# Optimization experiments

Hardware: AMD Instinct MI355X
Metric: run time of the kernel (lower is better)

The kernel has to match this reference:

```python
import jax, jax.numpy as jnp
import numpy as np
from jax import lax

T, I, H = 8192, 1024, 1024


def setup_inputs() -> dict:
    key = jax.random.key(0)
    ks = jax.random.split(key, 7)
    s = 1.0 / np.sqrt(H)
    x = jax.random.normal(ks[0], (T, I), dtype=jnp.float32)
    W_ih = jax.random.uniform(ks[1], (4 * H, I), minval=-s, maxval=s, dtype=jnp.float32)
    W_hh = jax.random.uniform(ks[2], (4 * H, H), minval=-s, maxval=s, dtype=jnp.float32)
    b_ih = jax.random.uniform(ks[3], (4 * H,), minval=-s, maxval=s, dtype=jnp.float32)
    b_hh = jax.random.uniform(ks[4], (4 * H,), minval=-s, maxval=s, dtype=jnp.float32)
    h0 = jax.random.normal(ks[5], (H,), dtype=jnp.float32)
    c0 = jax.random.uniform(ks[6], (H,), dtype=jnp.float32)
    return {"x": x, "W_ih": W_ih, "W_hh": W_hh, "b_ih": b_ih, "b_hh": b_hh, "h0": h0, "c0": c0}


def reference(x, W_ih, W_hh, b_ih, b_hh, h0, c0):
    # Precompute the input contribution to all gates in one big GEMM: [T, 4H]
    gates_x = x @ W_ih.T + (b_ih + b_hh)

    def step(carry, gx):
        h, c = carry
        g = gx + h @ W_hh.T  # [4H]
        i, f, gc, o = jnp.split(g, 4)  # PyTorch gate order: input, forget, cell, output
        i = jax.nn.sigmoid(i)
        f = jax.nn.sigmoid(f)
        gc = jnp.tanh(gc)
        o = jax.nn.sigmoid(o)
        c_new = f * c + i * gc
        h_new = o * jnp.tanh(c_new)
        return (h_new, c_new), h_new

    (_, _), hs = lax.scan(step, (h0, c0), gates_x)
    return hs  # [T, H] — the per-timestep outputs collected in fullDataOutput
```

## Files before the change

kernel.cpp:

```cpp
#include <hip/hip_runtime.h>
#include <cstdint>

#define T_STEPS 8192
#define HDIM    1024
#define NBLK    256
#define NTHR    256

typedef float        f32x4 __attribute__((ext_vector_type(4)));
typedef unsigned int u32x4 __attribute__((ext_vector_type(4)));

__device__ __forceinline__ float dot4(f32x4 a, f32x4 b) {
    return a[0] * b[0] + a[1] * b[1] + a[2] * b[2] + a[3] * b[3];
}
__device__ __forceinline__ float sigmoidf_(float v) { return 1.0f / (1.0f + __expf(-v)); }
__device__ __forceinline__ float tanhf_(float v)    { return 1.0f - 2.0f / (__expf(2.0f * v) + 1.0f); }
__device__ __forceinline__ unsigned bf16_rne(float f) {
    unsigned b = __float_as_uint(f);
    return (b + 0x7FFFu + ((b >> 16) & 1u)) >> 16;
}

__global__ __launch_bounds__(NTHR, 1)
void lstm_persistent(const float* __restrict__ x,
                     const float* __restrict__ W_ih,
                     const float* __restrict__ W_hh,
                     const float* __restrict__ b_ih,
                     const float* __restrict__ b_hh,
                     const float* __restrict__ h0,
                     const float* __restrict__ c0,
                     float* __restrict__ out,
                     unsigned int* __restrict__ ring)
{
    __shared__ float h_lds[2][HDIM];

    const int tid = threadIdx.x;
    const int w   = tid >> 6;
    const int l   = tid & 63;
    const int u   = (blockIdx.x << 2) + w;

    f32x4 whh[16], wih[16];
#pragma unroll
    for (int q = 0; q < 4; ++q) {
        const float* rh = W_hh + (size_t)(q * HDIM + u) * HDIM + 4 * l;
        const float* ri = W_ih + (size_t)(q * HDIM + u) * HDIM + 4 * l;
#pragma unroll
        for (int i = 0; i < 4; ++i) {
            whh[q * 4 + i] = *(const f32x4*)(rh + 256 * i);
            wih[q * 4 + i] = *(const f32x4*)(ri + 256 * i);
        }
    }
#pragma unroll
    for (int k = 0; k < 16; ++k) {
        asm volatile("" : "+v"(whh[k]));
        asm volatile("" : "+v"(wih[k]));
    }

    float bias[4];
#pragma unroll
    for (int q = 0; q < 4; ++q) bias[q] = b_ih[q * HDIM + u] + b_hh[q * HDIM + u];
    float c = c0[u];

    f32x4 hr[4];
#pragma unroll
    for (int i = 0; i < 4; ++i) hr[i] = *(const f32x4*)(h0 + 4 * l + 256 * i);

    float gxp[4];
    {
        f32x4 x0[4];
#pragma unroll
        for (int i = 0; i < 4; ++i) x0[i] = *(const f32x4*)(x + 4 * l + 256 * i);
#pragma unroll
        for (int q = 0; q < 4; ++q) {
            float a = 0.f;
#pragma unroll
            for (int i = 0; i < 4; ++i) a += dot4(wih[q * 4 + i], x0[i]);
            gxp[q] = a;
        }
    }
    f32x4 xr[4], xn[4];
#pragma unroll
    for (int i = 0; i < 4; ++i) xr[i] = *(const f32x4*)(x + HDIM + 4 * l + 256 * i);

    for (int t = 0; t < T_STEPS; ++t) {
        float acc[4];
#pragma unroll
        for (int q = 0; q < 4; ++q) {
            float a = gxp[q];
#pragma unroll
            for (int i = 0; i < 4; ++i) a += dot4(whh[q * 4 + i], hr[i]);
            acc[q] = a;
        }
#pragma unroll
        for (int m = 1; m < 64; m <<= 1) {
#pragma unroll
            for (int q = 0; q < 4; ++q) acc[q] += __shfl_xor(acc[q], m, 64);
        }
        const float gi = sigmoidf_(acc[0] + bias[0]);
        const float gf = sigmoidf_(acc[1] + bias[1]);
        const float gg = tanhf_   (acc[2] + bias[2]);
        const float go = sigmoidf_(acc[3] + bias[3]);
        c = gf * c + gi * gg;
        const float hval = go * tanhf_(c);

        if (l == 0) {
            const unsigned pk = ((unsigned)(t + 1) << 16) | bf16_rne(hval);
            unsigned int* slot =
                ring + (((t & 1) * NBLK + blockIdx.x) << 4) + w;
            asm volatile("global_store_dword %0, %1, off sc0 sc1"
                         :: "v"((unsigned long long)slot), "v"(pk) : "memory");
            out[(size_t)t * HDIM + u] = hval;
        }
        if (t == T_STEPS - 1) break;

        {
            const int tn = (t + 2 < T_STEPS) ? (t + 2) : (T_STEPS - 1);
            const float* xp = x + (size_t)tn * HDIM;
#pragma unroll
            for (int i = 0; i < 4; ++i) xn[i] = *(const f32x4*)(xp + 4 * l + 256 * i);
        }
#pragma unroll
        for (int q = 0; q < 4; ++q) {
            float a = 0.f;
#pragma unroll
            for (int i = 0; i < 4; ++i) a += dot4(wih[q * 4 + i], xr[i]);
            gxp[q] = a;
        }

        {
            const unsigned e = (unsigned)(t + 1);
            const unsigned long long base =
                (unsigned long long)(ring + (((t & 1) * NBLK + tid) << 4));
            u32x4 p;
            for (;;) {
                asm volatile(
                    "global_load_dwordx4 %0, %1, off sc0 sc1\n\t"
                    "s_waitcnt vmcnt(0)"
                    : "=&v"(p)
                    : "v"(base)
                    : "memory");
                if ((p[0] >> 16) == e && (p[1] >> 16) == e &&
                    (p[2] >> 16) == e && (p[3] >> 16) == e) break;
            }
            const int ns = (t + 1) & 1;
            f32x4 hv;
            hv[0] = __uint_as_float(p[0] << 16);
            hv[1] = __uint_as_float(p[1] << 16);
            hv[2] = __uint_as_float(p[2] << 16);
            hv[3] = __uint_as_float(p[3] << 16);
            *(f32x4*)&h_lds[ns][4 * tid] = hv;
        }
        __syncthreads();
        {
            const int ns = (t + 1) & 1;
#pragma unroll
            for (int i = 0; i < 4; ++i)
                hr[i] = *(const f32x4*)&h_lds[ns][4 * l + 256 * i];
        }
#pragma unroll
        for (int i = 0; i < 4; ++i) xr[i] = xn[i];
    }
}

extern "C" void kernel_launch(void* const* d_in, const int* in_sizes, int n_in,
                              void* d_out, int out_size, void* d_ws, size_t ws_size,
                              hipStream_t stream)
{
    const float* x    = (const float*)d_in[0];
    const float* W_ih = (const float*)d_in[1];
    const float* W_hh = (const float*)d_in[2];
    const float* b_ih = (const float*)d_in[3];
    const float* b_hh = (const float*)d_in[4];
    const float* h0   = (const float*)d_in[5];
    const float* c0   = (const float*)d_in[6];

    unsigned int* ring = (unsigned int*)d_ws;
    hipMemsetAsync(d_ws, 0, 2 * NBLK * 16 * sizeof(unsigned int), stream);
    lstm_persistent<<<NBLK, NTHR, 0, stream>>>(x, W_ih, W_hh, b_ih, b_hh, h0, c0,
                                               (float*)d_out, ring);
}
```

Measured before the change: 22.27 ms.

## Add dedicated polling wave per block to gather hidden state, overlapping compute waves

Adds a fifth wavefront to each block that alone polls the global ring buffer for the other blocks' hidden values, issuing four dwordx4 loads per lane and sleeping briefly between polls. The four compute waves no longer poll and only compute the input projection for the next step before the barrier. This separates synchronization latency from compute and aims to cut polling traffic from 256 threads to 64 per block. The output store moves to lane 1 so it does not share a lane with the ring store. The cost is an extra wave and a serial dependency on one polling wave, whose s_sleep may add latency on the critical path.

```diff
diff --git a/kernel.cpp b/kernel.cpp
--- a/kernel.cpp
+++ b/kernel.cpp
@@ -4,7 +4,7 @@
 #define T_STEPS 8192
 #define HDIM    1024
 #define NBLK    256
-#define NTHR    256
+#define NTHR    320
 
 typedef float        f32x4 __attribute__((ext_vector_type(4)));
 typedef unsigned int u32x4 __attribute__((ext_vector_type(4)));
@@ -38,125 +38,151 @@
     const int u   = (blockIdx.x << 2) + w;
 
     f32x4 whh[16], wih[16];
-#pragma unroll
-    for (int q = 0; q < 4; ++q) {
-        const float* rh = W_hh + (size_t)(q * HDIM + u) * HDIM + 4 * l;
-        const float* ri = W_ih + (size_t)(q * HDIM + u) * HDIM + 4 * l;
-#pragma unroll
-        for (int i = 0; i < 4; ++i) {
-            whh[q * 4 + i] = *(const f32x4*)(rh + 256 * i);
-            wih[q * 4 + i] = *(const f32x4*)(ri + 256 * i);
-        }
+    float bias[4] = {};
+    float c = 0.f;
+    f32x4 hr[4] = {};
+    float gxp[4] = {};
+    f32x4 xr[4] = {}, xn[4] = {};
+
+    if (w < 4) {
+#pragma unroll
+        for (int q = 0; q < 4; ++q) {
+            const float* rh = W_hh + (size_t)(q * HDIM + u) * HDIM + 4 * l;
+            const float* ri = W_ih + (size_t)(q * HDIM + u) * HDIM + 4 * l;
+#pragma unroll
+            for (int i = 0; i < 4; ++i) {
+                whh[q * 4 + i] = *(const f32x4*)(rh + 256 * i);
+                wih[q * 4 + i] = *(const f32x4*)(ri + 256 * i);
+            }
+        }
+#pragma unroll
+        for (int k = 0; k < 16; ++k) {
+            asm volatile("" : "+v"(whh[k]));
+            asm volatile("" : "+v"(wih[k]));
+        }
+#pragma unroll
+        for (int q = 0; q < 4; ++q) bias[q] = b_ih[q * HDIM + u] + b_hh[q * HDIM + u];
+        c = c0[u];
+#pragma unroll
+        for (int i = 0; i < 4; ++i) hr[i] = *(const f32x4*)(h0 + 4 * l + 256 * i);
+        {
+            f32x4 x0[4];
+#pragma unroll
+            for (int i = 0; i < 4; ++i) x0[i] = *(const f32x4*)(x + 4 * l + 256 * i);
+#pragma unroll
+            for (int q = 0; q < 4; ++q) {
+                float a = 0.f;
+#pragma unroll
+                for (int i = 0; i < 4; ++i) a += dot4(wih[q * 4 + i], x0[i]);
+                gxp[q] = a;
+            }
+        }
+#pragma unroll
+        for (int i = 0; i < 4; ++i) xr[i] = *(const f32x4*)(x + HDIM + 4 * l + 256 * i);
     }
-#pragma unroll
-    for (int k = 0; k < 16; ++k) {
-        asm volatile("" : "+v"(whh[k]));
-        asm volatile("" : "+v"(wih[k]));
-    }
-
-    float bias[4];
-#pragma unroll
-    for (int q = 0; q < 4; ++q) bias[q] = b_ih[q * HDIM + u] + b_hh[q * HDIM + u];
-    float c = c0[u];
-
-    f32x4 hr[4];
-#pragma unroll
-    for (int i = 0; i < 4; ++i) hr[i] = *(const f32x4*)(h0 + 4 * l + 256 * i);
-
-    float gxp[4];
-    {
-        f32x4 x0[4];
-#pragma unroll
-        for (int i = 0; i < 4; ++i) x0[i] = *(const f32x4*)(x + 4 * l + 256 * i);
-#pragma unroll
-        for (int q = 0; q < 4; ++q) {
-            float a = 0.f;
-#pragma unroll
-            for (int i = 0; i < 4; ++i) a += dot4(wih[q * 4 + i], x0[i]);
-            gxp[q] = a;
-        }
-    }
-    f32x4 xr[4], xn[4];
-#pragma unroll
-    for (int i = 0; i < 4; ++i) xr[i] = *(const f32x4*)(x + HDIM + 4 * l + 256 * i);
+
+    const unsigned long long ringb = (unsigned long long)ring;
 
     for (int t = 0; t < T_STEPS; ++t) {
-        float acc[4];
-#pragma unroll
-        for (int q = 0; q < 4; ++q) {
-            float a = gxp[q];
-#pragma unroll
-            for (int i = 0; i < 4; ++i) a += dot4(whh[q * 4 + i], hr[i]);
-            acc[q] = a;
-        }
-#pragma unroll
-        for (int m = 1; m < 64; m <<= 1) {
-#pragma unroll
-            for (int q = 0; q < 4; ++q) acc[q] += __shfl_xor(acc[q], m, 64);
-        }
-        const float gi = sigmoidf_(acc[0] + bias[0]);
-        const float gf = sigmoidf_(acc[1] + bias[1]);
-        const float gg = tanhf_   (acc[2] + bias[2]);
-        const float go = sigmoidf_(acc[3] + bias[3]);
-        c = gf * c + gi * gg;
-        const float hval = go * tanhf_(c);
-
-        if (l == 0) {
-            const unsigned pk = ((unsigned)(t + 1) << 16) | bf16_rne(hval);
-            unsigned int* slot =
-                ring + (((t & 1) * NBLK + blockIdx.x) << 4) + w;
-            asm volatile("global_store_dword %0, %1, off sc0 sc1"
-                         :: "v"((unsigned long long)slot), "v"(pk) : "memory");
-            out[(size_t)t * HDIM + u] = hval;
+        if (w < 4) {
+            float acc[4];
+#pragma unroll
+            for (int q = 0; q < 4; ++q) {
+                float a = gxp[q];
+#pragma unroll
+                for (int i = 0; i < 4; ++i) a += dot4(whh[q * 4 + i], hr[i]);
+                acc[q] = a;
+            }
+#pragma unroll
+            for (int m = 1; m < 64; m <<= 1) {
+#pragma unroll
+                for (int q = 0; q < 4; ++q) acc[q] += __shfl_xor(acc[q], m, 64);
+            }
+            const float gi = sigmoidf_(acc[0] + bias[0]);
+            const float gf = sigmoidf_(acc[1] + bias[1]);
+            const float gg = tanhf_   (acc[2] + bias[2]);
+            const float go = sigmoidf_(acc[3] + bias[3]);
+            c = gf * c + gi * gg;
+            const float hval = go * tanhf_(c);
+
+            if (l == 0) {
+                const unsigned pk = ((unsigned)(t + 1) << 16) | bf16_rne(hval);
+                unsigned int* slot =
+                    ring + (((t & 1) * NBLK + blockIdx.x) << 4) + w;
+                asm volatile("global_store_dword %0, %1, off sc0 sc1"
+                             :: "v"((unsigned long long)slot), "v"(pk) : "memory");
+            }
+            if (l == 1) out[(size_t)t * HDIM + u] = hval;
         }
         if (t == T_STEPS - 1) break;
 
-        {
+        if (w < 4) {
             const int tn = (t + 2 < T_STEPS) ? (t + 2) : (T_STEPS - 1);
             const float* xp = x + (size_t)tn * HDIM;
 #pragma unroll
             for (int i = 0; i < 4; ++i) xn[i] = *(const f32x4*)(xp + 4 * l + 256 * i);
-        }
-#pragma unroll
-        for (int q = 0; q < 4; ++q) {
-            float a = 0.f;
-#pragma unroll
-            for (int i = 0; i < 4; ++i) a += dot4(wih[q * 4 + i], xr[i]);
-            gxp[q] = a;
-        }
-
-        {
+#pragma unroll
+            for (int q = 0; q < 4; ++q) {
+                float a = 0.f;
+#pragma unroll
+                for (int i = 0; i < 4; ++i) a += dot4(wih[q * 4 + i], xr[i]);
+                gxp[q] = a;
+            }
+        } else {
             const unsigned e = (unsigned)(t + 1);
-            const unsigned long long base =
-                (unsigned long long)(ring + (((t & 1) * NBLK + tid) << 4));
-            u32x4 p;
+            const unsigned long long pb =
+                ringb + (unsigned long long)((t & 1) * 16384 + (l << 6));
+            const unsigned long long a0 = pb;
+            const unsigned long long a1 = pb + 4096;
+            const unsigned long long a2 = pb + 8192;
+            const unsigned long long a3 = pb + 12288;
+            u32x4 p0, p1, p2, p3;
             for (;;) {
                 asm volatile(
-                    "global_load_dwordx4 %0, %1, off sc0 sc1\n\t"
+                    "global_load_dwordx4 %0, %4, off sc0 sc1\n\t"
+                    "global_load_dwordx4 %1, %5, off sc0 sc1\n\t"
+                    "global_load_dwordx4 %2, %6, off sc0 sc1\n\t"
+                    "global_load_dwordx4 %3, %7, off sc0 sc1\n\t"
                     "s_waitcnt vmcnt(0)"
-                    : "=&v"(p)
-                    : "v"(base)
+                    : "=&v"(p0), "=&v"(p1), "=&v"(p2), "=&v"(p3)
+                    : "v"(a0), "v"(a1), "v"(a2), "v"(a3)
                     : "memory");
-                if ((p[0] >> 16) == e && (p[1] >> 16) == e &&
-                    (p[2] >> 16) == e && (p[3] >> 16) == e) break;
+                const bool ok =
+                    (p0[0] >> 16) == e && (p0[1] >> 16) == e &&
+                    (p0[2] >> 16) == e && (p0[3] >> 16) == e &&
+                    (p1[0] >> 16) == e && (p1[1] >> 16) == e &&
+                    (p1[2] >> 16) == e && (p1[3] >> 16) == e &&
+                    (p2[0] >> 16) == e && (p2[1] >> 16) == e &&
+                    (p2[2] >> 16) == e && (p2[3] >> 16) == e &&
+                    (p3[0] >> 16) == e && (p3[1] >> 16) == e &&
+                    (p3[2] >> 16) == e && (p3[3] >> 16) == e;
+                if (ok) break;
+                __builtin_amdgcn_s_sleep(1);
             }
             const int ns = (t + 1) & 1;
             f32x4 hv;
-            hv[0] = __uint_as_float(p[0] << 16);
-            hv[1] = __uint_as_float(p[1] << 16);
-            hv[2] = __uint_as_float(p[2] << 16);
-            hv[3] = __uint_as_float(p[3] << 16);
-            *(f32x4*)&h_lds[ns][4 * tid] = hv;
+#pragma unroll
+            for (int j = 0; j < 4; ++j) hv[j] = __uint_as_float(p0[j] << 16);
+            *(f32x4*)&h_lds[ns][4 * l] = hv;
+#pragma unroll
+            for (int j = 0; j < 4; ++j) hv[j] = __uint_as_float(p1[j] << 16);
+            *(f32x4*)&h_lds[ns][4 * l + 256] = hv;
+#pragma unroll
+            for (int j = 0; j < 4; ++j) hv[j] = __uint_as_float(p2[j] << 16);
+            *(f32x4*)&h_lds[ns][4 * l + 512] = hv;
+#pragma unroll
+            for (int j = 0; j < 4; ++j) hv[j] = __uint_as_float(p3[j] << 16);
+            *(f32x4*)&h_lds[ns][4 * l + 768] = hv;
         }
         __syncthreads();
-        {
+        if (w < 4) {
             const int ns = (t + 1) & 1;
 #pragma unroll
             for (int i = 0; i < 4; ++i)
                 hr[i] = *(const f32x4*)&h_lds[ns][4 * l + 256 * i];
-        }
-#pragma unroll
-        for (int i = 0; i < 4; ++i) xr[i] = xn[i];
+#pragma unroll
+            for (int i = 0; i < 4; ++i) xr[i] = xn[i];
+        }
     }
 }
 
```

New measurement: 26.65 ms. 1.2x slower.

## Split each hidden unit's dot product across two wave halves with dedicated pollers

Applied to the files above, without the earlier changes.

Doubles the block to 512 threads so each hidden unit's K dimension is split between two waves, halving per-thread weight registers and per-step FMA work. The second-half waves combine partial sums through LDS and take over ring polling and h broadcast, while the first-half waves compute gates and publish h. Per-step outputs go to a per-block staging buffer and a separate untranspose kernel writes the final [T,H] layout. This adds an extra barrier per step, an LDS exchange and a second kernel launch.

```diff
diff --git a/kernel.cpp b/kernel.cpp
--- a/kernel.cpp
+++ b/kernel.cpp
@@ -4,7 +4,6 @@
 #define T_STEPS 8192
 #define HDIM    1024
 #define NBLK    256
-#define NTHR    256
 
 typedef float        f32x4 __attribute__((ext_vector_type(4)));
 typedef unsigned int u32x4 __attribute__((ext_vector_type(4)));
@@ -19,7 +18,14 @@
     return (b + 0x7FFFu + ((b >> 16) & 1u)) >> 16;
 }
 
-__global__ __launch_bounds__(NTHR, 1)
+#define BAR() do {                                            \
+    asm volatile("s_waitcnt lgkmcnt(0)" ::: "memory");        \
+    __builtin_amdgcn_sched_barrier(0);                        \
+    __builtin_amdgcn_s_barrier();                             \
+    __builtin_amdgcn_sched_barrier(0);                        \
+} while (0)
+
+__global__ __launch_bounds__(512, 2)
 void lstm_persistent(const float* __restrict__ x,
                      const float* __restrict__ W_ih,
                      const float* __restrict__ W_hh,
@@ -27,137 +33,146 @@
                      const float* __restrict__ b_hh,
                      const float* __restrict__ h0,
                      const float* __restrict__ c0,
-                     float* __restrict__ out,
+                     float* __restrict__ stag,
                      unsigned int* __restrict__ ring)
 {
     __shared__ float h_lds[2][HDIM];
+    __shared__ float p_lds[4][4];
 
     const int tid = threadIdx.x;
     const int w   = tid >> 6;
     const int l   = tid & 63;
-    const int u   = (blockIdx.x << 2) + w;
+    const int r   = w & 3;
+    const int hh  = w >> 2;
+    const int u   = (blockIdx.x << 2) + r;
+    const int koff = 4 * l + 512 * hh;
 
-    f32x4 whh[16], wih[16];
+    f32x4 whh[8], wih[8];
 #pragma unroll
     for (int q = 0; q < 4; ++q) {
-        const float* rh = W_hh + (size_t)(q * HDIM + u) * HDIM + 4 * l;
-        const float* ri = W_ih + (size_t)(q * HDIM + u) * HDIM + 4 * l;
-#pragma unroll
-        for (int i = 0; i < 4; ++i) {
-            whh[q * 4 + i] = *(const f32x4*)(rh + 256 * i);
-            wih[q * 4 + i] = *(const f32x4*)(ri + 256 * i);
-        }
-    }
-#pragma unroll
-    for (int k = 0; k < 16; ++k) {
-        asm volatile("" : "+v"(whh[k]));
-        asm volatile("" : "+v"(wih[k]));
+        const float* rh = W_hh + (size_t)(q * HDIM + u) * HDIM + koff;
+        const float* ri = W_ih + (size_t)(q * HDIM + u) * HDIM + koff;
+        whh[q * 2 + 0] = *(const f32x4*)(rh);
+        whh[q * 2 + 1] = *(const f32x4*)(rh + 256);
+        wih[q * 2 + 0] = *(const f32x4*)(ri);
+        wih[q * 2 + 1] = *(const f32x4*)(ri + 256);
     }
 
-    float bias[4];
+    float bias[4] = {};
+    float c = 0.f;
+    if (w < 4) {
 #pragma unroll
-    for (int q = 0; q < 4; ++q) bias[q] = b_ih[q * HDIM + u] + b_hh[q * HDIM + u];
-    float c = c0[u];
+        for (int q = 0; q < 4; ++q) bias[q] = b_ih[q * HDIM + u] + b_hh[q * HDIM + u];
+        c = c0[u];
+    }
 
-    f32x4 hr[4];
+    f32x4 hrh[2];
+    hrh[0] = *(const f32x4*)(h0 + koff);
+    hrh[1] = *(const f32x4*)(h0 + koff + 256);
+
+    float gxpp[4];
+    {
+        f32x4 x0h0 = *(const f32x4*)(x + koff);
+        f32x4 x0h1 = *(const f32x4*)(x + koff + 256);
 #pragma unroll
-    for (int i = 0; i < 4; ++i) hr[i] = *(const f32x4*)(h0 + 4 * l + 256 * i);
+        for (int q = 0; q < 4; ++q)
+            gxpp[q] = dot4(wih[q * 2], x0h0) + dot4(wih[q * 2 + 1], x0h1);
+    }
+    f32x4 xrh[2], xnh[2];
+    xrh[0] = *(const f32x4*)(x + HDIM + koff);
+    xrh[1] = *(const f32x4*)(x + HDIM + koff + 256);
 
-    float gxp[4];
-    {
-        f32x4 x0[4];
-#pragma unroll
-        for (int i = 0; i < 4; ++i) x0[i] = *(const f32x4*)(x + 4 * l + 256 * i);
-#pragma unroll
-        for (int q = 0; q < 4; ++q) {
-            float a = 0.f;
-#pragma unroll
-            for (int i = 0; i < 4; ++i) a += dot4(wih[q * 4 + i], x0[i]);
-            gxp[q] = a;
-        }
-    }
-    f32x4 xr[4], xn[4];
-#pragma unroll
-    for (int i = 0; i < 4; ++i) xr[i] = *(const f32x4*)(x + HDIM + 4 * l + 256 * i);
+    float* stagb = stag + (size_t)blockIdx.x * T_STEPS * 4;
 
     for (int t = 0; t < T_STEPS; ++t) {
         float acc[4];
 #pragma unroll
-        for (int q = 0; q < 4; ++q) {
-            float a = gxp[q];
-#pragma unroll
-            for (int i = 0; i < 4; ++i) a += dot4(whh[q * 4 + i], hr[i]);
-            acc[q] = a;
-        }
+        for (int q = 0; q < 4; ++q)
+            acc[q] = gxpp[q] + dot4(whh[q * 2], hrh[0]) + dot4(whh[q * 2 + 1], hrh[1]);
 #pragma unroll
         for (int m = 1; m < 64; m <<= 1) {
 #pragma unroll
             for (int q = 0; q < 4; ++q) acc[q] += __shfl_xor(acc[q], m, 64);
         }
-        const float gi = sigmoidf_(acc[0] + bias[0]);
-        const float gf = sigmoidf_(acc[1] + bias[1]);
-        const float gg = tanhf_   (acc[2] + bias[2]);
-        const float go = sigmoidf_(acc[3] + bias[3]);
-        c = gf * c + gi * gg;
-        const float hval = go * tanhf_(c);
+        if (w >= 4 && l == 0) {
+            f32x4 pv; pv[0] = acc[0]; pv[1] = acc[1]; pv[2] = acc[2]; pv[3] = acc[3];
+            *(f32x4*)&p_lds[r][0] = pv;
+        }
+        BAR();
 
-        if (l == 0) {
-            const unsigned pk = ((unsigned)(t + 1) << 16) | bf16_rne(hval);
-            unsigned int* slot =
-                ring + (((t & 1) * NBLK + blockIdx.x) << 4) + w;
-            asm volatile("global_store_dword %0, %1, off sc0 sc1"
-                         :: "v"((unsigned long long)slot), "v"(pk) : "memory");
-            out[(size_t)t * HDIM + u] = hval;
+        const int tn = (t + 2 < T_STEPS) ? (t + 2) : (T_STEPS - 1);
+        const float* xp = x + (size_t)tn * HDIM + koff;
+
+        if (w < 4) {
+            const f32x4 part = *(const f32x4*)&p_lds[r][0];
+            const float gi = sigmoidf_(acc[0] + part[0] + bias[0]);
+            const float gf = sigmoidf_(acc[1] + part[1] + bias[1]);
+            const float gg = tanhf_   (acc[2] + part[2] + bias[2]);
+            const float go = sigmoidf_(acc[3] + part[3] + bias[3]);
+            c = gf * c + gi * gg;
+            const float hval = go * tanhf_(c);
+
+            if (l == 0) {
+                const unsigned pk = ((unsigned)(t + 1) << 16) | bf16_rne(hval);
+                unsigned int* slot =
+                    ring + (((t & 1) * NBLK + blockIdx.x) << 4) + r;
+                asm volatile("global_store_dword %0, %1, off sc0 sc1"
+                             :: "v"((unsigned long long)slot), "v"(pk) : "memory");
+            }
+            if (l == 1) stagb[t * 4 + r] = hval;
+
+            xnh[0] = *(const f32x4*)(xp);
+            xnh[1] = *(const f32x4*)(xp + 256);
+#pragma unroll
+            for (int q = 0; q < 4; ++q)
+                gxpp[q] = dot4(wih[q * 2], xrh[0]) + dot4(wih[q * 2 + 1], xrh[1]);
+        } else {
+#pragma unroll
+            for (int q = 0; q < 4; ++q)
+                gxpp[q] = dot4(wih[q * 2], xrh[0]) + dot4(wih[q * 2 + 1], xrh[1]);
+            if (t < T_STEPS - 1) {
+                const int p_idx = ((w - 4) << 6) + l;
+                const unsigned e = (unsigned)(t + 1);
+                const unsigned long long base =
+                    (unsigned long long)(ring + (((t & 1) * NBLK + p_idx) << 4));
+                u32x4 p;
+                for (;;) {
+                    asm volatile(
+                        "global_load_dwordx4 %0, %1, off sc0 sc1\n\t"
+                        "s_waitcnt vmcnt(0)"
+                        : "=&v"(p) : "v"(base));
+                    if ((p[0] >> 16) == e && (p[1] >> 16) == e &&
+                        (p[2] >> 16) == e && (p[3] >> 16) == e) break;
+                }
+                const int ns = (t + 1) & 1;
+                f32x4 hv;
+                hv[0] = __uint_as_float(p[0] << 16);
+                hv[1] = __uint_as_float(p[1] << 16);
+                hv[2] = __uint_as_float(p[2] << 16);
+                hv[3] = __uint_as_float(p[3] << 16);
+                *(f32x4*)&h_lds[ns][4 * p_idx] = hv;
+                xnh[0] = *(const f32x4*)(xp);
+                xnh[1] = *(const f32x4*)(xp + 256);
+            }
         }
         if (t == T_STEPS - 1) break;
-
-        {
-            const int tn = (t + 2 < T_STEPS) ? (t + 2) : (T_STEPS - 1);
-            const float* xp = x + (size_t)tn * HDIM;
-#pragma unroll
-            for (int i = 0; i < 4; ++i) xn[i] = *(const f32x4*)(xp + 4 * l + 256 * i);
-        }
-#pragma unroll
-        for (int q = 0; q < 4; ++q) {
-            float a = 0.f;
-#pragma unroll
-            for (int i = 0; i < 4; ++i) a += dot4(wih[q * 4 + i], xr[i]);
-            gxp[q] = a;
-        }
-
-        {
-            const unsigned e = (unsigned)(t + 1);
-            const unsigned long long base =
-                (unsigned long long)(ring + (((t & 1) * NBLK + tid) << 4));
-            u32x4 p;
-            for (;;) {
-                asm volatile(
-                    "global_load_dwordx4 %0, %1, off sc0 sc1\n\t"
-                    "s_waitcnt vmcnt(0)"
-                    : "=&v"(p)
-                    : "v"(base)
-                    : "memory");
-                if ((p[0] >> 16) == e && (p[1] >> 16) == e &&
-                    (p[2] >> 16) == e && (p[3] >> 16) == e) break;
-            }
-            const int ns = (t + 1) & 1;
-            f32x4 hv;
-            hv[0] = __uint_as_float(p[0] << 16);
-            hv[1] = __uint_as_float(p[1] << 16);
-            hv[2] = __uint_as_float(p[2] << 16);
-            hv[3] = __uint_as_float(p[3] << 16);
-            *(f32x4*)&h_lds[ns][4 * tid] = hv;
-        }
-        __syncthreads();
+        BAR();
         {
             const int ns = (t + 1) & 1;
-#pragma unroll
-            for (int i = 0; i < 4; ++i)
-                hr[i] = *(const f32x4*)&h_lds[ns][4 * l + 256 * i];
+            hrh[0] = *(const f32x4*)&h_lds[ns][koff];
+            hrh[1] = *(const f32x4*)&h_lds[ns][koff + 256];
         }
-#pragma unroll
-        for (int i = 0; i < 4; ++i) xr[i] = xn[i];
+        xrh[0] = xnh[0]; xrh[1] = xnh[1];
     }
+}
+
+__global__ __launch_bounds__(256)
+void untranspose(const float* __restrict__ stag, float* __restrict__ out)
+{
+    const int t = blockIdx.x;
+    const int b = threadIdx.x;
+    f32x4 v = *(const f32x4*)(stag + (size_t)b * T_STEPS * 4 + t * 4);
+    *(f32x4*)(out + (size_t)t * HDIM + 4 * b) = v;
 }
 
 extern "C" void kernel_launch(void* const* d_in, const int* in_sizes, int n_in,
@@ -173,7 +188,10 @@
     const float* c0   = (const float*)d_in[6];
 
     unsigned int* ring = (unsigned int*)d_ws;
+    float* stag = (float*)((char*)d_ws + (1u << 20));
+
     hipMemsetAsync(d_ws, 0, 2 * NBLK * 16 * sizeof(unsigned int), stream);
-    lstm_persistent<<<NBLK, NTHR, 0, stream>>>(x, W_ih, W_hh, b_ih, b_hh, h0, c0,
-                                               (float*)d_out, ring);
+    lstm_persistent<<<NBLK, 512, 0, stream>>>(x, W_ih, W_hh, b_ih, b_hh, h0, c0,
+                                              stag, ring);
+    untranspose<<<T_STEPS, 256, 0, stream>>>(stag, (float*)d_out);
 }
```

Result: slower. 33.56 ms (+50.7%).

## Replace shuffle reduction with DPP and drop LDS exchange barrier

Applied to the files above, without the earlier changes.

The butterfly shuffle reduction is replaced by a DPP row_shr/row_bcast reduction, with the result read from lane 63. Each wave now polls all four ring segments itself and unpacks h straight into registers, which removes the shared-memory staging and the __syncthreads barrier. The output store moves after the poll so it stays off the critical path. The cost is four times more polling traffic per wave on the global ring, spread over four loads.

```diff
diff --git a/kernel.cpp b/kernel.cpp
--- a/kernel.cpp
+++ b/kernel.cpp
@@ -17,6 +17,22 @@
 __device__ __forceinline__ unsigned bf16_rne(float f) {
     unsigned b = __float_as_uint(f);
     return (b + 0x7FFFu + ((b >> 16) & 1u)) >> 16;
+}
+
+__device__ __forceinline__ float red64(float v) {
+    v += __int_as_float(__builtin_amdgcn_update_dpp(
+            0, __float_as_int(v), 0x111, 0xF, 0xF, false));
+    v += __int_as_float(__builtin_amdgcn_update_dpp(
+            0, __float_as_int(v), 0x112, 0xF, 0xF, false));
+    v += __int_as_float(__builtin_amdgcn_update_dpp(
+            0, __float_as_int(v), 0x114, 0xF, 0xF, false));
+    v += __int_as_float(__builtin_amdgcn_update_dpp(
+            0, __float_as_int(v), 0x118, 0xF, 0xF, false));
+    v += __int_as_float(__builtin_amdgcn_update_dpp(
+            0, __float_as_int(v), 0x142, 0xF, 0xF, false));
+    v += __int_as_float(__builtin_amdgcn_update_dpp(
+            0, __float_as_int(v), 0x143, 0xF, 0xF, false));
+    return v;
 }
 
 __global__ __launch_bounds__(NTHR, 1)
@@ -30,8 +46,6 @@
                      float* __restrict__ out,
                      unsigned int* __restrict__ ring)
 {
-    __shared__ float h_lds[2][HDIM];
-
     const int tid = threadIdx.x;
     const int w   = tid >> 6;
     const int l   = tid & 63;
@@ -80,6 +94,8 @@
 #pragma unroll
     for (int i = 0; i < 4; ++i) xr[i] = *(const f32x4*)(x + HDIM + 4 * l + 256 * i);
 
+    const unsigned long long ringb = (unsigned long long)ring;
+
     for (int t = 0; t < T_STEPS; ++t) {
         float acc[4];
 #pragma unroll
@@ -87,12 +103,7 @@
             float a = gxp[q];
 #pragma unroll
             for (int i = 0; i < 4; ++i) a += dot4(whh[q * 4 + i], hr[i]);
-            acc[q] = a;
-        }
-#pragma unroll
-        for (int m = 1; m < 64; m <<= 1) {
-#pragma unroll
-            for (int q = 0; q < 4; ++q) acc[q] += __shfl_xor(acc[q], m, 64);
+            acc[q] = red64(a);
         }
         const float gi = sigmoidf_(acc[0] + bias[0]);
         const float gf = sigmoidf_(acc[1] + bias[1]);
@@ -101,15 +112,16 @@
         c = gf * c + gi * gg;
         const float hval = go * tanhf_(c);
 
-        if (l == 0) {
+        if (l == 63) {
             const unsigned pk = ((unsigned)(t + 1) << 16) | bf16_rne(hval);
-            unsigned int* slot =
-                ring + (((t & 1) * NBLK + blockIdx.x) << 4) + w;
+            unsigned int* slot = ring + (((t & 1) * NBLK + blockIdx.x) << 4) + w;
             asm volatile("global_store_dword %0, %1, off sc0 sc1"
                          :: "v"((unsigned long long)slot), "v"(pk) : "memory");
-            out[(size_t)t * HDIM + u] = hval;
-        }
-        if (t == T_STEPS - 1) break;
+        }
+        if (t == T_STEPS - 1) {
+            if (l == 63) out[(size_t)t * HDIM + u] = hval;
+            break;
+        }
 
         {
             const int tn = (t + 2 < T_STEPS) ? (t + 2) : (T_STEPS - 1);
@@ -127,34 +139,43 @@
 
         {
             const unsigned e = (unsigned)(t + 1);
-            const unsigned long long base =
-                (unsigned long long)(ring + (((t & 1) * NBLK + tid) << 4));
-            u32x4 p;
+            const unsigned long long a0 =
+                ringb + (unsigned long long)((t & 1) * 16384 + (l << 6));
+            const unsigned long long a1 = a0 + 4096;
+            const unsigned long long a2 = a0 + 8192;
+            const unsigned long long a3 = a0 + 12288;
+            u32x4 p0, p1, p2, p3;
             for (;;) {
                 asm volatile(
-                    "global_load_dwordx4 %0, %1, off sc0 sc1\n\t"
+                    "global_load_dwordx4 %0, %4, off sc0 sc1\n\t"
+                    "global_load_dwordx4 %1, %5, off sc0 sc1\n\t"
+                    "global_load_dwordx4 %2, %6, off sc0 sc1\n\t"
+                    "global_load_dwordx4 %3, %7, off sc0 sc1\n\t"
                     "s_waitcnt vmcnt(0)"
-                    : "=&v"(p)
-                    : "v"(base)
+                    : "=&v"(p0), "=&v"(p1), "=&v"(p2), "=&v"(p3)
+                    : "v"(a0), "v"(a1), "v"(a2), "v"(a3)
                     : "memory");
-                if ((p[0] >> 16) == e && (p[1] >> 16) == e &&
-                    (p[2] >> 16) == e && (p[3] >> 16) == e) break;
+                unsigned bad = (p0[0] >> 16) ^ e;
+                bad |= (p0[1] >> 16) ^ e;  bad |= (p0[2] >> 16) ^ e;
+                bad |= (p0[3] >> 16) ^ e;  bad |= (p1[0] >> 16) ^ e;
+                bad |= (p1[1] >> 16) ^ e;  bad |= (p1[2] >> 16) ^ e;
+                bad |= (p1[3] >> 16) ^ e;  bad |= (p2[0] >> 16) ^ e;
+                bad |= (p2[1] >> 16) ^ e;  bad |= (p2[2] >> 16) ^ e;
+                bad |= (p2[3] >> 16) ^ e;  bad |= (p3[0] >> 16) ^ e;
+                bad |= (p3[1] >> 16) ^ e;  bad |= (p3[2] >> 16) ^ e;
+                bad |= (p3[3] >> 16) ^ e;
+                if (bad == 0u) break;
             }
-            const int ns = (t + 1) & 1;
-            f32x4 hv;
-            hv[0] = __uint_as_float(p[0] << 16);
-            hv[1] = __uint_as_float(p[1] << 16);
-            hv[2] = __uint_as_float(p[2] << 16);
-            hv[3] = __uint_as_float(p[3] << 16);
-            *(f32x4*)&h_lds[ns][4 * tid] = hv;
-        }
-        __syncthreads();
-        {
-            const int ns = (t + 1) & 1;
-#pragma unroll
-            for (int i = 0; i < 4; ++i)
-                hr[i] = *(const f32x4*)&h_lds[ns][4 * l + 256 * i];
-        }
+#pragma unroll
+            for (int j = 0; j < 4; ++j) hr[0][j] = __uint_as_float(p0[j] << 16);
+#pragma unroll
+            for (int j = 0; j < 4; ++j) hr[1][j] = __uint_as_float(p1[j] << 16);
+#pragma unroll
+            for (int j = 0; j < 4; ++j) hr[2][j] = __uint_as_float(p2[j] << 16);
+#pragma unroll
+            for (int j = 0; j < 4; ++j) hr[3][j] = __uint_as_float(p3[j] << 16);
+        }
+        if (l == 63) out[(size_t)t * HDIM + u] = hval;
 #pragma unroll
         for (int i = 0; i < 4; ++i) xr[i] = xn[i];
     }
```

Result: slower. 40.33 ms (+81.1%).
